# Kernel tuning notes

Hardware: AMD Instinct MI355X
Metric: run time of the kernel (lower is better)

Reference implementation:

```python
import jax, jax.numpy as jnp
import numpy as np

B, R, D, P = 32, 512, 256, 5532  # images, rois/image, feat dim, num_pids
NEG_INF = -1e30

def setup_inputs() -> dict:
    key = jax.random.key(0)
    k1, k2, k3 = jax.random.split(key, 3)
    inputs = jax.random.normal(k1, (B * R, D), dtype=jnp.float32)
    cls_scores = jax.random.uniform(k2, (B * R, 1), dtype=jnp.float32)
    roi_label = jax.random.randint(k3, (B, R), 0, P + 1)  # 0 = background -> label -1
    return {"inputs": inputs, "cls_scores": cls_scores, "roi_label": roi_label}

def reference(inputs, cls_scores, roi_label):
    x = (inputs * cls_scores).reshape(B, R, D)          # scale features by cls score
    label = roi_label - 1                               # [B,R], -1 = background
    valid = label >= 0                                  # keep labeled ROIs only
    lbl = jnp.where(valid, label, 0)

    # per-image per-pid mean prototypes via one segmented reduction
    seg = (jnp.arange(B)[:, None] * P + lbl).reshape(-1)             # [B*R]
    w = valid.reshape(-1).astype(x.dtype)
    sums = jax.ops.segment_sum(x.reshape(-1, D) * w[:, None], seg, num_segments=B * P)
    counts = jax.ops.segment_sum(w, seg, num_segments=B * P)          # [B*P]
    proto = sums / jnp.maximum(counts, 1.0)[:, None]
    proto = proto / jnp.maximum(jnp.linalg.norm(proto, axis=-1, keepdims=True), 1e-12)
    proto = jax.lax.stop_gradient(proto).reshape(B, P, D)            # .detach() in torch
    present = (counts > 0).reshape(B, P)                              # unique labels per image

    # project each ROI feature onto its image's prototypes
    logits = jnp.einsum('brd,bpd->brp', x, proto)                     # [B,R,P]
    logits = jnp.where(present[:, None, :], logits, NEG_INF)          # softmax over unique labels only
    logp = jax.nn.log_softmax(logits, axis=-1)
    nll = -jnp.take_along_axis(logp, lbl[..., None], axis=-1)[..., 0] # [B,R]
    nll = jnp.where(valid, nll, 0.0)
    n_valid = jnp.maximum(jnp.sum(valid).astype(x.dtype), 1.0)
    return jnp.sum(nll) / n_valid
```

## Files before the change

### kernel.cpp

```cpp
#include <hip/hip_runtime.h>
#include <math.h>

#define Bn 32
#define Rn 512
#define Dn 256
#define Pn 5532
#define MAXU 512

typedef short short8 __attribute__((ext_vector_type(8)));
typedef short short4v __attribute__((ext_vector_type(4)));
typedef float floatx4 __attribute__((ext_vector_type(4)));

#define XBF_OFF    0
#define XBF_WORDS  (Bn*Rn*Dn/2)
#define PBF_OFF    (XBF_OFF + XBF_WORDS)
#define PBF_WORDS  (Bn*MAXU*Dn/2)
#define LBLC_OFF   (PBF_OFF + PBF_WORDS)
#define CCNT_OFF   (LBLC_OFF + Bn*Rn)
#define CURS_OFF   (CCNT_OFF + Bn*MAXU)
#define RLIST_OFF  (CURS_OFF + Bn*MAXU)
#define NUNIQ_OFF  (RLIST_OFF + Bn*Rn)
#define NVALID_OFF (NUNIQ_OFF + 32)
#define NLL_OFF    (NVALID_OFF + 32)
#define TICK_OFF   (NLL_OFF + 1)
#define ZEROW      2

__device__ __forceinline__ unsigned short bf16r(float f) {
    union { float f; unsigned int u; } c; c.f = f;
    return (unsigned short)((c.u + 0x7FFFu + ((c.u >> 16) & 1u)) >> 16);
}
__device__ __forceinline__ float bfu2f(unsigned int hi16) {
    union { unsigned int u; float f; } c; c.u = hi16;
    return c.f;
}

__device__ __forceinline__ void async16(void* lds, const void* g) {
    auto* l3 = reinterpret_cast<__attribute__((address_space(3))) unsigned int*>(
                   reinterpret_cast<size_t>(lds));
    auto* g1 = reinterpret_cast<const __attribute__((address_space(1))) unsigned int*>(
                   reinterpret_cast<size_t>(g));
    __builtin_amdgcn_global_load_lds(g1, l3, 16, 0, 0);
}

__global__ __launch_bounds__(1024) void k1_prep(
    const float* __restrict__ inputs, const float* __restrict__ cls,
    const int* __restrict__ roi_label,
    unsigned short* __restrict__ xbf,
    int* __restrict__ lblc_arr, int* __restrict__ ccnt, int* __restrict__ cursor,
    int* __restrict__ rlist, int* __restrict__ nuniq, int* __restrict__ nvalid_arr,
    int* __restrict__ zbase)
{
    const int flat = blockIdx.x;
    const int t = threadIdx.x;

    __shared__ int cnt_lds[Pn];
    __shared__ int cmap_lds[Pn];
    __shared__ int curs_lds[MAXU];
    __shared__ int wpres[16], wcnt[16];

    if (flat >= 32) {
        if (flat == 33 && t < ZEROW) zbase[t] = 0;
        int g = (flat - 32) * 1024 + t;
        int e = g * 8;
        int row = e >> 8;
        float cw = cls[row];
        float4 v0 = *(const float4*)&inputs[e];
        float4 v1 = *(const float4*)&inputs[e + 4];
        short8 o;
        o[0] = (short)bf16r(v0.x * cw); o[1] = (short)bf16r(v0.y * cw);
        o[2] = (short)bf16r(v0.z * cw); o[3] = (short)bf16r(v0.w * cw);
        o[4] = (short)bf16r(v1.x * cw); o[5] = (short)bf16r(v1.y * cw);
        o[6] = (short)bf16r(v1.z * cw); o[7] = (short)bf16r(v1.w * cw);
        *(short8*)&xbf[e] = o;
        return;
    }

    const int b = flat;
    const int lane = t & 63, wid = t >> 6;
    for (int i = t; i < Pn; i += 1024) cnt_lds[i] = 0;
    __syncthreads();
    int mylbl = -1;
    if (t < Rn) {
        mylbl = roi_label[b * Rn + t] - 1;
        if (mylbl >= 0) atomicAdd(&cnt_lds[mylbl], 1);
    }
    __syncthreads();

    int basePres = 0, baseCnt = 0;
    for (int i0 = 0; i0 < Pn; i0 += 1024) {
        int i = i0 + t;
        int cnt = (i < Pn) ? cnt_lds[i] : 0;
        bool pres = cnt > 0;
        unsigned long long mask = __ballot(pres);
        int pfx_pres = __popcll(mask & ((1ULL << lane) - 1ULL));
        int v = cnt;
        #pragma unroll
        for (int off = 1; off < 64; off <<= 1) {
            int u = __shfl_up(v, off);
            if (lane >= off) v += u;
        }
        int pfx_cnt = v - cnt;
        if (lane == 63) { wpres[wid] = __popcll(mask); wcnt[wid] = v; }
        __syncthreads();
        int woffP = 0, totP = 0, woffC = 0, totC = 0;
        #pragma unroll
        for (int w = 0; w < 16; ++w) {
            int p = wpres[w], c = wcnt[w];
            if (w < wid) { woffP += p; woffC += c; }
            totP += p; totC += c;
        }
        if (pres) {
            int c = basePres + woffP + pfx_pres;
            cmap_lds[i] = c;
            ccnt[b * MAXU + c] = cnt;
            curs_lds[c] = baseCnt + woffC + pfx_cnt;
        }
        basePres += totP; baseCnt += totC;
        __syncthreads();
    }
    if (t < Rn) {
        int lc = (mylbl >= 0) ? cmap_lds[mylbl] : -1;
        lblc_arr[b * Rn + t] = lc;
        if (lc >= 0) {
            int pos = atomicAdd(&curs_lds[lc], 1);
            rlist[b * Rn + pos] = t;
        }
    }
    __syncthreads();
    if (t < MAXU && t < basePres)
        cursor[b * MAXU + t] = curs_lds[t];
    if (t == 0) { nuniq[b] = basePres; nvalid_arr[b] = baseCnt; }
}

__global__ __launch_bounds__(256) void k2_proto(
    const unsigned short* __restrict__ xbf,
    const int* __restrict__ nuniq, const int* __restrict__ ccnt,
    const int* __restrict__ cursor, const int* __restrict__ rlist,
    unsigned short* __restrict__ pbf)
{
    const int lane = threadIdx.x & 63, wv = threadIdx.x >> 6;
    int s = blockIdx.x * 4 + wv;
    int b = s >> 9;
    int c = s & (MAXU - 1);
    if (c >= nuniq[b]) return;
    int cnt = ccnt[s];
    int start = cursor[s] - cnt;
    float a0 = 0.f, a1 = 0.f, a2 = 0.f, a3 = 0.f;
    for (int k = 0; k < cnt; ++k) {
        int r = rlist[b * Rn + start + k];
        uint2 pk = *(const uint2*)&xbf[((size_t)(b * Rn + r)) * Dn + lane * 4];
        a0 += bfu2f(pk.x << 16); a1 += bfu2f(pk.x & 0xFFFF0000u);
        a2 += bfu2f(pk.y << 16); a3 += bfu2f(pk.y & 0xFFFF0000u);
    }
    float inv = 1.0f / (float)cnt;
    a0 *= inv; a1 *= inv; a2 *= inv; a3 *= inv;
    float ss = a0*a0 + a1*a1 + a2*a2 + a3*a3;
    #pragma unroll
    for (int off = 32; off > 0; off >>= 1) ss += __shfl_xor(ss, off);
    float scale = 1.0f / fmaxf(sqrtf(ss), 1e-12f);
    short4v o;
    o[0] = (short)bf16r(a0 * scale); o[1] = (short)bf16r(a1 * scale);
    o[2] = (short)bf16r(a2 * scale); o[3] = (short)bf16r(a3 * scale);
    *(short4v*)&pbf[(size_t)s * Dn + lane * 4] = o;
}

#define TRr 32
#define TCc 128
#define KCs 64
#define NSTG (Dn / KCs)
#define NBLK ((Rn / TRr) * Bn)

__global__ __launch_bounds__(256, 3) void k3_loss(
    const unsigned short* __restrict__ xbf, const unsigned short* __restrict__ pbf,
    const int* __restrict__ lblc_arr, const int* __restrict__ nuniq,
    const int* __restrict__ nvalid_arr,
    float* __restrict__ nll, int* __restrict__ tick, float* __restrict__ out)
{
    __shared__ __align__(16) unsigned short xs[TRr * Dn];
    __shared__ __align__(16) unsigned short ps[2][TCc * KCs];
    __shared__ int lblc[TRr];
    __shared__ float esum_lds[4][TRr];
    __shared__ float dsum_lds[4][TRr];

    const int t = threadIdx.x;
    const int lane = t & 63, w = t >> 6;
    const int q = lane >> 4, r15 = lane & 15;
    const int rt = blockIdx.x;
    const int b  = blockIdx.y;
    const int roiBase = rt * TRr;
    const int U = nuniq[b];
    const int nch = (U <= 0) ? 1 : ((U + TCc - 1) >> 7);

    if (t < TRr) lblc[t] = lblc_arr[b * Rn + roiBase + t];

    #pragma unroll
    for (int i = 0; i < 4; ++i) {
        int ci = i * 256 + w * 64 + lane;
        int row = ci >> 5, gpos = ci & 31;
        int g = gpos ^ (row & 7);
        async16(&xs[(i * 256 + w * 64) * 8],
                xbf + (size_t)(b * Rn + roiBase + row) * Dn + g * 8);
    }

#define ISSUE_PS(PC, ST, BUF)                                                \
    do {                                                                     \
        _Pragma("unroll")                                                    \
        for (int i_ = 0; i_ < 4; ++i_) {                                     \
            int ci_ = i_ * 256 + w * 64 + lane;                              \
            int pr_ = ci_ >> 3, gp_ = ci_ & 7;                               \
            int g_ = gp_ ^ (pr_ & 7);                                        \
            async16(&ps[BUF][(i_ * 256 + w * 64) * 8],                       \
                    pbf + (size_t)(b * MAXU + (PC) * TCc + pr_) * Dn         \
                        + (ST) * KCs + g_ * 8);                              \
        }                                                                    \
    } while (0)

    ISSUE_PS(0, 0, 0);
    __syncthreads();

    short8 areg[2][8];
    #pragma unroll
    for (int mt = 0; mt < 2; ++mt)
        #pragma unroll
        for (int kcs = 0; kcs < 8; ++kcs) {
            int row = mt * 16 + r15;
            int gpos = (kcs * 4 + q) ^ (row & 7);
            areg[mt][kcs] = *(const short8*)&xs[row * Dn + gpos * 8];
        }

    int lcr[2][4];
    float esum[2][4], dsum[2][4];
    #pragma unroll
    for (int mt = 0; mt < 2; ++mt)
        #pragma unroll
        for (int reg = 0; reg < 4; ++reg) {
            lcr[mt][reg] = lblc[mt * 16 + q * 4 + reg];
            esum[mt][reg] = 0.f; dsum[mt][reg] = 0.f;
        }

    for (int pc = 0; pc < nch; ++pc) {
        floatx4 acc[2][2];
        #pragma unroll
        for (int mt = 0; mt < 2; ++mt) {
            acc[mt][0] = (floatx4)0.f; acc[mt][1] = (floatx4)0.f;
        }

        #pragma unroll
        for (int st = 0; st < NSTG; ++st) {
            const int cur = st & 1;
            __syncthreads();
            int ns = pc * NSTG + st + 1;
            if (ns < nch * NSTG) ISSUE_PS(ns >> 2, ns & 3, cur ^ 1);
            #pragma unroll
            for (int kk = 0; kk < 2; ++kk) {
                short8 bb[2];
                #pragma unroll
                for (int nt = 0; nt < 2; ++nt) {
                    int r = w * 32 + nt * 16 + r15;
                    int gpos = (kk * 4 + q) ^ (r & 7);
                    bb[nt] = *(const short8*)&ps[cur][r * KCs + gpos * 8];
                }
                #pragma unroll
                for (int mt = 0; mt < 2; ++mt) {
                    acc[mt][0] = __builtin_amdgcn_mfma_f32_16x16x32_bf16(
                        areg[mt][st * 2 + kk], bb[0], acc[mt][0], 0, 0, 0);
                    acc[mt][1] = __builtin_amdgcn_mfma_f32_16x16x32_bf16(
                        areg[mt][st * 2 + kk], bb[1], acc[mt][1], 0, 0, 0);
                }
            }
        }

        #pragma unroll
        for (int nt = 0; nt < 2; ++nt) {
            int c = pc * TCc + w * 32 + nt * 16 + r15;
            bool v = c < U;
            #pragma unroll
            for (int mt = 0; mt < 2; ++mt)
                #pragma unroll
                for (int reg = 0; reg < 4; ++reg) {
                    float d = acc[mt][nt][reg];
                    if (v) esum[mt][reg] += __expf(d);
                    if (c == lcr[mt][reg]) dsum[mt][reg] += d;
                }
        }
    }
#undef ISSUE_PS

    #pragma unroll
    for (int mt = 0; mt < 2; ++mt)
        #pragma unroll
        for (int reg = 0; reg < 4; ++reg) {
            float e = esum[mt][reg], d = dsum[mt][reg];
            #pragma unroll
            for (int off = 1; off < 16; off <<= 1) {
                e += __shfl_xor(e, off);
                d += __shfl_xor(d, off);
            }
            if (r15 == 0) {
                int row = mt * 16 + q * 4 + reg;
                esum_lds[w][row] = e;
                dsum_lds[w][row] = d;
            }
        }
    __syncthreads();
    if (t < TRr) {
        float es = esum_lds[0][t] + esum_lds[1][t] + esum_lds[2][t] + esum_lds[3][t];
        float ds = dsum_lds[0][t] + dsum_lds[1][t] + dsum_lds[2][t] + dsum_lds[3][t];
        float val = (lblc[t] >= 0) ? (__logf(es) - ds) : 0.f;
        #pragma unroll
        for (int off = 1; off < 32; off <<= 1) val += __shfl_xor(val, off);
        if (t == 0) {
            atomicAdd(nll, val);
            __threadfence();
            int old = atomicAdd(tick, 1);
            if (old == NBLK - 1) {
                float total = atomicAdd(nll, 0.0f);
                int nv = 0;
                #pragma unroll
                for (int i = 0; i < Bn / 4; ++i) {
                    int4 vv = ((const int4*)nvalid_arr)[i];
                    nv += vv.x + vv.y + vv.z + vv.w;
                }
                out[0] = total / fmaxf((float)nv, 1.0f);
            }
        }
    }
}

extern "C" void kernel_launch(void* const* d_in, const int* in_sizes, int n_in,
                              void* d_out, int out_size, void* d_ws, size_t ws_size,
                              hipStream_t stream) {
    const float* inputs = (const float*)d_in[0];
    const float* cls    = (const float*)d_in[1];
    const int*   roi    = (const int*)d_in[2];
    float* out = (float*)d_out;

    float* wsf = (float*)d_ws;
    int*   wsi = (int*)d_ws;
    unsigned short* xbf = (unsigned short*)(wsi + XBF_OFF);
    unsigned short* pbf = (unsigned short*)(wsi + PBF_OFF);
    int*   lblc   = wsi + LBLC_OFF;
    int*   ccnt   = wsi + CCNT_OFF;
    int*   cursor = wsi + CURS_OFF;
    int*   rlist  = wsi + RLIST_OFF;
    int*   nuniq  = wsi + NUNIQ_OFF;
    int*   nvalid = wsi + NVALID_OFF;
    float* nll    = wsf + NLL_OFF;
    int*   tick   = wsi + TICK_OFF;

    k1_prep<<<32 + 512, 1024, 0, stream>>>(inputs, cls, roi, xbf, lblc, ccnt,
                                           cursor, rlist, nuniq, nvalid,
                                           wsi + NLL_OFF);
    k2_proto<<<(Bn * MAXU) / 4, 256, 0, stream>>>(xbf, nuniq, ccnt, cursor,
                                                  rlist, pbf);
    dim3 g(Rn / TRr, Bn);
    k3_loss<<<g, 256, 0, stream>>>(xbf, pbf, lblc, nuniq, nvalid, nll, tick, out);
}
```

Before: 104.9 us.

## Fuse prep, prototype and loss kernels into one persistent kernel with grid barriers

Merges the three launches into a single persistent kernel of 512 blocks. Stages are separated by a software grid barrier built on atomics. The bf16 scaled-feature buffer is no longer written to global memory: prototypes and loss tiles recompute the cls-scaled bf16 values straight from the fp32 inputs. Label compaction now assigns slots by first-arrival atomics instead of a prefix scan over all pids. This removes launch gaps and the intermediate round trip, at the cost of barrier spin overhead, a co-residency requirement for all 512 blocks, and only 32 blocks doing the prep stage.

Result: slower. 191.3 us (+82.4%).

```diff
diff --git a/kernel.cpp b/kernel.cpp
--- a/kernel.cpp
+++ b/kernel.cpp
@@ -6,14 +6,15 @@
 #define Dn 256
 #define Pn 5532
 #define MAXU 512
-
-typedef short short8 __attribute__((ext_vector_type(8)));
-typedef short short4v __attribute__((ext_vector_type(4)));
-typedef float floatx4 __attribute__((ext_vector_type(4)));
-
-#define XBF_OFF    0
-#define XBF_WORDS  (Bn*Rn*Dn/2)
-#define PBF_OFF    (XBF_OFF + XBF_WORDS)
+#define GRID 512
+
+#define TRr 32
+#define TCc 128
+#define KCs 64
+#define NSTG (Dn / KCs)
+#define NBLK GRID
+
+#define PBF_OFF    0
 #define PBF_WORDS  (Bn*MAXU*Dn/2)
 #define LBLC_OFF   (PBF_OFF + PBF_WORDS)
 #define CCNT_OFF   (LBLC_OFF + Bn*Rn)
@@ -23,7 +24,11 @@
 #define NVALID_OFF (NUNIQ_OFF + 32)
 #define NLL_OFF    (NVALID_OFF + 32)
 #define TICK_OFF   (NLL_OFF + 1)
-#define ZEROW      2
+#define BAR_OFF    (TICK_OFF + 1)
+
+typedef short short8 __attribute__((ext_vector_type(8)));
+typedef short short4v __attribute__((ext_vector_type(4)));
+typedef float floatx4 __attribute__((ext_vector_type(4)));
 
 __device__ __forceinline__ unsigned short bf16r(float f) {
     union { float f; unsigned int u; } c; c.f = f;
@@ -42,165 +47,161 @@
     __builtin_amdgcn_global_load_lds(g1, l3, 16, 0, 0);
 }
 
-__global__ __launch_bounds__(1024) void k1_prep(
-    const float* __restrict__ inputs, const float* __restrict__ cls,
-    const int* __restrict__ roi_label,
-    unsigned short* __restrict__ xbf,
-    int* __restrict__ lblc_arr, int* __restrict__ ccnt, int* __restrict__ cursor,
-    int* __restrict__ rlist, int* __restrict__ nuniq, int* __restrict__ nvalid_arr,
-    int* __restrict__ zbase)
-{
-    const int flat = blockIdx.x;
-    const int t = threadIdx.x;
-
-    __shared__ int cnt_lds[Pn];
-    __shared__ int cmap_lds[Pn];
-    __shared__ int curs_lds[MAXU];
-    __shared__ int wpres[16], wcnt[16];
-
-    if (flat >= 32) {
-        if (flat == 33 && t < ZEROW) zbase[t] = 0;
-        int g = (flat - 32) * 1024 + t;
-        int e = g * 8;
-        int row = e >> 8;
-        float cw = cls[row];
-        float4 v0 = *(const float4*)&inputs[e];
-        float4 v1 = *(const float4*)&inputs[e + 4];
-        short8 o;
-        o[0] = (short)bf16r(v0.x * cw); o[1] = (short)bf16r(v0.y * cw);
-        o[2] = (short)bf16r(v0.z * cw); o[3] = (short)bf16r(v0.w * cw);
-        o[4] = (short)bf16r(v1.x * cw); o[5] = (short)bf16r(v1.y * cw);
-        o[6] = (short)bf16r(v1.z * cw); o[7] = (short)bf16r(v1.w * cw);
-        *(short8*)&xbf[e] = o;
-        return;
-    }
-
-    const int b = flat;
-    const int lane = t & 63, wid = t >> 6;
-    for (int i = t; i < Pn; i += 1024) cnt_lds[i] = 0;
+__device__ __forceinline__ void gbar(int* bar, int target) {
     __syncthreads();
-    int mylbl = -1;
-    if (t < Rn) {
-        mylbl = roi_label[b * Rn + t] - 1;
-        if (mylbl >= 0) atomicAdd(&cnt_lds[mylbl], 1);
+    if (threadIdx.x == 0) {
+        __threadfence();
+        atomicAdd(bar, 1);
+        while (atomicAdd(bar, 0) < target)
+            __builtin_amdgcn_s_sleep(8);
+        __threadfence();
     }
     __syncthreads();
-
-    int basePres = 0, baseCnt = 0;
-    for (int i0 = 0; i0 < Pn; i0 += 1024) {
-        int i = i0 + t;
-        int cnt = (i < Pn) ? cnt_lds[i] : 0;
-        bool pres = cnt > 0;
-        unsigned long long mask = __ballot(pres);
-        int pfx_pres = __popcll(mask & ((1ULL << lane) - 1ULL));
-        int v = cnt;
-        #pragma unroll
-        for (int off = 1; off < 64; off <<= 1) {
-            int u = __shfl_up(v, off);
-            if (lane >= off) v += u;
-        }
-        int pfx_cnt = v - cnt;
-        if (lane == 63) { wpres[wid] = __popcll(mask); wcnt[wid] = v; }
-        __syncthreads();
-        int woffP = 0, totP = 0, woffC = 0, totC = 0;
-        #pragma unroll
-        for (int w = 0; w < 16; ++w) {
-            int p = wpres[w], c = wcnt[w];
-            if (w < wid) { woffP += p; woffC += c; }
-            totP += p; totC += c;
-        }
-        if (pres) {
-            int c = basePres + woffP + pfx_pres;
-            cmap_lds[i] = c;
-            ccnt[b * MAXU + c] = cnt;
-            curs_lds[c] = baseCnt + woffC + pfx_cnt;
-        }
-        basePres += totP; baseCnt += totC;
-        __syncthreads();
+}
+
+__global__ __launch_bounds__(256, 2) void fused(
+    const float* __restrict__ inputs, const float* __restrict__ cls,
+    const int* __restrict__ roi_label, int* __restrict__ wsi,
+    float* __restrict__ out)
+{
+    __shared__ __align__(16) char smem[50432];
+
+    const int t = threadIdx.x;
+    const int blk = blockIdx.x;
+    const int lane = t & 63, wv = t >> 6;
+
+    unsigned short* pbf = (unsigned short*)(wsi + PBF_OFF);
+    int* lblc_arr = wsi + LBLC_OFF;
+    int* ccnt     = wsi + CCNT_OFF;
+    int* cursor   = wsi + CURS_OFF;
+    int* rlist    = wsi + RLIST_OFF;
+    int* nuniq    = wsi + NUNIQ_OFF;
+    int* nvalid_a = wsi + NVALID_OFF;
+    float* nll    = (float*)(wsi + NLL_OFF);
+    int* tick     = wsi + TICK_OFF;
+    int* bar      = wsi + BAR_OFF;
+
+    if (blk < Bn) {
+        int* cnt_l  = (int*)smem;
+        int* slot_l = cnt_l + Pn;
+        int* scnt   = slot_l + Pn;
+        int* sbase  = scnt + MAXU;
+        int* scur   = sbase + MAXU;
+        int* ctrs   = scur + MAXU;
+        const int b = blk;
+        for (int i = t; i < Pn; i += 256) cnt_l[i] = 0;
+        for (int i = t; i < MAXU; i += 256) scnt[i] = 0;
+        if (t == 0) ctrs[0] = 0;
+        __syncthreads();
+        int myl[2], mylc[2];
+        #pragma unroll
+        for (int j = 0; j < 2; ++j) {
+            int l = roi_label[b * Rn + t + j * 256] - 1;
+            myl[j] = l;
+            if (l >= 0) {
+                if (atomicAdd(&cnt_l[l], 1) == 0)
+                    slot_l[l] = atomicAdd(&ctrs[0], 1);
+            }
+        }
+        __syncthreads();
+        #pragma unroll
+        for (int j = 0; j < 2; ++j) {
+            int lc = (myl[j] >= 0) ? slot_l[myl[j]] : -1;
+            mylc[j] = lc;
+            lblc_arr[b * Rn + t + j * 256] = lc;
+            if (lc >= 0) atomicAdd(&scnt[lc], 1);
+        }
+        __syncthreads();
+        const int U = ctrs[0];
+        int base = 0;
+        for (int i0 = 0; i0 < MAXU; i0 += 256) {
+            int v = scnt[i0 + t], vs = v;
+            #pragma unroll
+            for (int off = 1; off < 64; off <<= 1) {
+                int u = __shfl_up(vs, off);
+                if (lane >= off) vs += u;
+            }
+            if (lane == 63) ctrs[2 + wv] = vs;
+            __syncthreads();
+            int woff = 0, tot = 0;
+            #pragma unroll
+            for (int w = 0; w < 4; ++w) {
+                int x = ctrs[2 + w];
+                if (w < wv) woff += x;
+                tot += x;
+            }
+            int st = base + woff + (vs - v);
+            sbase[i0 + t] = st;
+            scur[i0 + t]  = st;
+            base += tot;
+            __syncthreads();
+        }
+        #pragma unroll
+        for (int j = 0; j < 2; ++j) {
+            int lc = mylc[j];
+            if (lc >= 0) {
+                int pos = atomicAdd(&scur[lc], 1);
+                rlist[b * Rn + pos] = t + j * 256;
+            }
+        }
+        __syncthreads();
+        for (int i = t; i < MAXU; i += 256)
+            if (i < U) { ccnt[b*MAXU+i] = scnt[i]; cursor[b*MAXU+i] = sbase[i]; }
+        if (t == 0) { nuniq[b] = U; nvalid_a[b] = base; }
     }
-    if (t < Rn) {
-        int lc = (mylbl >= 0) ? cmap_lds[mylbl] : -1;
-        lblc_arr[b * Rn + t] = lc;
-        if (lc >= 0) {
-            int pos = atomicAdd(&curs_lds[lc], 1);
-            rlist[b * Rn + pos] = t;
+
+    gbar(bar, GRID);
+
+    {
+        const int gs0 = blk * 32 + wv * 8;
+        const int b = gs0 >> 9;
+        const int Ub = nuniq[b];
+        for (int i = 0; i < 8; ++i) {
+            int c = (gs0 + i) & (MAXU - 1);
+            if (c >= Ub) continue;
+            int s = b * MAXU + c;
+            int cnt = ccnt[s], start = cursor[s];
+            float a0 = 0.f, a1 = 0.f, a2 = 0.f, a3 = 0.f;
+            for (int k = 0; k < cnt; ++k) {
+                int row = b * Rn + rlist[b * Rn + start + k];
+                float cw = cls[row];
+                float4 v = *(const float4*)&inputs[(size_t)row * Dn + lane * 4];
+                a0 += bfu2f(((unsigned)bf16r(v.x * cw)) << 16);
+                a1 += bfu2f(((unsigned)bf16r(v.y * cw)) << 16);
+                a2 += bfu2f(((unsigned)bf16r(v.z * cw)) << 16);
+                a3 += bfu2f(((unsigned)bf16r(v.w * cw)) << 16);
+            }
+            float inv = 1.0f / (float)cnt;
+            a0 *= inv; a1 *= inv; a2 *= inv; a3 *= inv;
+            float ss = a0*a0 + a1*a1 + a2*a2 + a3*a3;
+            #pragma unroll
+            for (int off = 32; off > 0; off >>= 1) ss += __shfl_xor(ss, off);
+            float sc = 1.0f / fmaxf(sqrtf(ss), 1e-12f);
+            short4v o;
+            o[0] = (short)bf16r(a0 * sc); o[1] = (short)bf16r(a1 * sc);
+            o[2] = (short)bf16r(a2 * sc); o[3] = (short)bf16r(a3 * sc);
+            *(short4v*)&pbf[(size_t)s * Dn + lane * 4] = o;
         }
     }
-    __syncthreads();
-    if (t < MAXU && t < basePres)
-        cursor[b * MAXU + t] = curs_lds[t];
-    if (t == 0) { nuniq[b] = basePres; nvalid_arr[b] = baseCnt; }
-}
-
-__global__ __launch_bounds__(256) void k2_proto(
-    const unsigned short* __restrict__ xbf,
-    const int* __restrict__ nuniq, const int* __restrict__ ccnt,
-    const int* __restrict__ cursor, const int* __restrict__ rlist,
-    unsigned short* __restrict__ pbf)
-{
-    const int lane = threadIdx.x & 63, wv = threadIdx.x >> 6;
-    int s = blockIdx.x * 4 + wv;
-    int b = s >> 9;
-    int c = s & (MAXU - 1);
-    if (c >= nuniq[b]) return;
-    int cnt = ccnt[s];
-    int start = cursor[s] - cnt;
-    float a0 = 0.f, a1 = 0.f, a2 = 0.f, a3 = 0.f;
-    for (int k = 0; k < cnt; ++k) {
-        int r = rlist[b * Rn + start + k];
-        uint2 pk = *(const uint2*)&xbf[((size_t)(b * Rn + r)) * Dn + lane * 4];
-        a0 += bfu2f(pk.x << 16); a1 += bfu2f(pk.x & 0xFFFF0000u);
-        a2 += bfu2f(pk.y << 16); a3 += bfu2f(pk.y & 0xFFFF0000u);
-    }
-    float inv = 1.0f / (float)cnt;
-    a0 *= inv; a1 *= inv; a2 *= inv; a3 *= inv;
-    float ss = a0*a0 + a1*a1 + a2*a2 + a3*a3;
-    #pragma unroll
-    for (int off = 32; off > 0; off >>= 1) ss += __shfl_xor(ss, off);
-    float scale = 1.0f / fmaxf(sqrtf(ss), 1e-12f);
-    short4v o;
-    o[0] = (short)bf16r(a0 * scale); o[1] = (short)bf16r(a1 * scale);
-    o[2] = (short)bf16r(a2 * scale); o[3] = (short)bf16r(a3 * scale);
-    *(short4v*)&pbf[(size_t)s * Dn + lane * 4] = o;
-}
-
-#define TRr 32
-#define TCc 128
-#define KCs 64
-#define NSTG (Dn / KCs)
-#define NBLK ((Rn / TRr) * Bn)
-
-__global__ __launch_bounds__(256, 3) void k3_loss(
-    const unsigned short* __restrict__ xbf, const unsigned short* __restrict__ pbf,
-    const int* __restrict__ lblc_arr, const int* __restrict__ nuniq,
-    const int* __restrict__ nvalid_arr,
-    float* __restrict__ nll, int* __restrict__ tick, float* __restrict__ out)
-{
-    __shared__ __align__(16) unsigned short xs[TRr * Dn];
-    __shared__ __align__(16) unsigned short ps[2][TCc * KCs];
-    __shared__ int lblc[TRr];
-    __shared__ float esum_lds[4][TRr];
-    __shared__ float dsum_lds[4][TRr];
-
-    const int t = threadIdx.x;
-    const int lane = t & 63, w = t >> 6;
-    const int q = lane >> 4, r15 = lane & 15;
-    const int rt = blockIdx.x;
-    const int b  = blockIdx.y;
-    const int roiBase = rt * TRr;
-    const int U = nuniq[b];
-    const int nch = (U <= 0) ? 1 : ((U + TCc - 1) >> 7);
-
-    if (t < TRr) lblc[t] = lblc_arr[b * Rn + roiBase + t];
-
-    #pragma unroll
-    for (int i = 0; i < 4; ++i) {
-        int ci = i * 256 + w * 64 + lane;
-        int row = ci >> 5, gpos = ci & 31;
-        int g = gpos ^ (row & 7);
-        async16(&xs[(i * 256 + w * 64) * 8],
-                xbf + (size_t)(b * Rn + roiBase + row) * Dn + g * 8);
-    }
+
+    gbar(bar, 2 * GRID);
+
+    {
+        unsigned short* xs  = (unsigned short*)smem;
+        unsigned short* psb = xs + TRr * Dn;
+        int*   lblc = (int*)(psb + 2 * TCc * KCs);
+        float* es_l = (float*)(lblc + TRr);
+        float* ds_l = es_l + 4 * TRr;
+
+        const int w = wv;
+        const int q = lane >> 4, r15 = lane & 15;
+        const int rt = blk & 15;
+        const int b  = blk >> 4;
+        const int roiBase = rt * TRr;
+        const int U = nuniq[b];
+        const int nch = (U <= 0) ? 1 : ((U + TCc - 1) >> 7);
+
+        if (t < TRr) lblc[t] = lblc_arr[b * Rn + roiBase + t];
 
 #define ISSUE_PS(PC, ST, BUF)                                                \
     do {                                                                     \
@@ -209,119 +210,140 @@
             int ci_ = i_ * 256 + w * 64 + lane;                              \
             int pr_ = ci_ >> 3, gp_ = ci_ & 7;                               \
             int g_ = gp_ ^ (pr_ & 7);                                        \
-            async16(&ps[BUF][(i_ * 256 + w * 64) * 8],                       \
+            async16(psb + (size_t)(BUF) * (TCc * KCs)                        \
+                        + (size_t)(i_ * 256 + w * 64) * 8,                   \
                     pbf + (size_t)(b * MAXU + (PC) * TCc + pr_) * Dn         \
                         + (ST) * KCs + g_ * 8);                              \
         }                                                                    \
     } while (0)
 
-    ISSUE_PS(0, 0, 0);
-    __syncthreads();
-
-    short8 areg[2][8];
-    #pragma unroll
-    for (int mt = 0; mt < 2; ++mt)
-        #pragma unroll
-        for (int kcs = 0; kcs < 8; ++kcs) {
-            int row = mt * 16 + r15;
-            int gpos = (kcs * 4 + q) ^ (row & 7);
-            areg[mt][kcs] = *(const short8*)&xs[row * Dn + gpos * 8];
-        }
-
-    int lcr[2][4];
-    float esum[2][4], dsum[2][4];
-    #pragma unroll
-    for (int mt = 0; mt < 2; ++mt)
-        #pragma unroll
-        for (int reg = 0; reg < 4; ++reg) {
-            lcr[mt][reg] = lblc[mt * 16 + q * 4 + reg];
-            esum[mt][reg] = 0.f; dsum[mt][reg] = 0.f;
-        }
-
-    for (int pc = 0; pc < nch; ++pc) {
-        floatx4 acc[2][2];
-        #pragma unroll
-        for (int mt = 0; mt < 2; ++mt) {
-            acc[mt][0] = (floatx4)0.f; acc[mt][1] = (floatx4)0.f;
-        }
-
-        #pragma unroll
-        for (int st = 0; st < NSTG; ++st) {
-            const int cur = st & 1;
-            __syncthreads();
-            int ns = pc * NSTG + st + 1;
-            if (ns < nch * NSTG) ISSUE_PS(ns >> 2, ns & 3, cur ^ 1);
-            #pragma unroll
-            for (int kk = 0; kk < 2; ++kk) {
-                short8 bb[2];
+        ISSUE_PS(0, 0, 0);
+
+        {
+            const int row = t >> 3, seg = t & 7;
+            const size_t gbase = (size_t)(b * Rn + roiBase + row) * Dn + seg * 32;
+            const float cw = cls[b * Rn + roiBase + row];
+            #pragma unroll
+            for (int jj = 0; jj < 4; ++jj) {
+                float4 v0 = *(const float4*)&inputs[gbase + jj * 8];
+                float4 v1 = *(const float4*)&inputs[gbase + jj * 8 + 4];
+                short8 o;
+                o[0] = (short)bf16r(v0.x * cw); o[1] = (short)bf16r(v0.y * cw);
+                o[2] = (short)bf16r(v0.z * cw); o[3] = (short)bf16r(v0.w * cw);
+                o[4] = (short)bf16r(v1.x * cw); o[5] = (short)bf16r(v1.y * cw);
+                o[6] = (short)bf16r(v1.z * cw); o[7] = (short)bf16r(v1.w * cw);
+                int gpos = (seg * 4 + jj) ^ (row & 7);
+                *(short8*)&xs[row * Dn + gpos * 8] = o;
+            }
+        }
+        __syncthreads();
+
+        short8 areg[2][8];
+        #pragma unroll
+        for (int mt = 0; mt < 2; ++mt)
+            #pragma unroll
+            for (int kcs = 0; kcs < 8; ++kcs) {
+                int row = mt * 16 + r15;
+                int gpos = (kcs * 4 + q) ^ (row & 7);
+                areg[mt][kcs] = *(const short8*)&xs[row * Dn + gpos * 8];
+            }
+
+        int lcr[2][4];
+        float esum[2][4], dsum[2][4];
+        #pragma unroll
+        for (int mt = 0; mt < 2; ++mt)
+            #pragma unroll
+            for (int reg = 0; reg < 4; ++reg) {
+                lcr[mt][reg] = lblc[mt * 16 + q * 4 + reg];
+                esum[mt][reg] = 0.f; dsum[mt][reg] = 0.f;
+            }
+
+        for (int pc = 0; pc < nch; ++pc) {
+            floatx4 acc[2][2];
+            #pragma unroll
+            for (int mt = 0; mt < 2; ++mt) {
+                acc[mt][0] = (floatx4)0.f; acc[mt][1] = (floatx4)0.f;
+            }
+
+            #pragma unroll
+            for (int st = 0; st < NSTG; ++st) {
+                const int cur = st & 1;
+                __syncthreads();
+                int ns = pc * NSTG + st + 1;
+                if (ns < nch * NSTG) ISSUE_PS(ns >> 2, ns & 3, cur ^ 1);
+                const unsigned short* pscur = psb + (size_t)cur * (TCc * KCs);
                 #pragma unroll
-                for (int nt = 0; nt < 2; ++nt) {
-                    int r = w * 32 + nt * 16 + r15;
-                    int gpos = (kk * 4 + q) ^ (r & 7);
-                    bb[nt] = *(const short8*)&ps[cur][r * KCs + gpos * 8];
+                for (int kk = 0; kk < 2; ++kk) {
+                    short8 bb[2];
+                    #pragma unroll
+                    for (int nt = 0; nt < 2; ++nt) {
+                        int r = w * 32 + nt * 16 + r15;
+                        int gpos = (kk * 4 + q) ^ (r & 7);
+                        bb[nt] = *(const short8*)&pscur[r * KCs + gpos * 8];
+                    }
+                    #pragma unroll
+                    for (int mt = 0; mt < 2; ++mt) {
+                        acc[mt][0] = __builtin_amdgcn_mfma_f32_16x16x32_bf16(
+                            areg[mt][st * 2 + kk], bb[0], acc[mt][0], 0, 0, 0);
+                        acc[mt][1] = __builtin_amdgcn_mfma_f32_16x16x32_bf16(
+                            areg[mt][st * 2 + kk], bb[1], acc[mt][1], 0, 0, 0);
+                    }
                 }
+            }
+
+            #pragma unroll
+            for (int nt = 0; nt < 2; ++nt) {
+                int c = pc * TCc + w * 32 + nt * 16 + r15;
+                bool v = c < U;
                 #pragma unroll
-                for (int mt = 0; mt < 2; ++mt) {
-                    acc[mt][0] = __builtin_amdgcn_mfma_f32_16x16x32_bf16(
-                        areg[mt][st * 2 + kk], bb[0], acc[mt][0], 0, 0, 0);
-                    acc[mt][1] = __builtin_amdgcn_mfma_f32_16x16x32_bf16(
-                        areg[mt][st * 2 + kk], bb[1], acc[mt][1], 0, 0, 0);
+                for (int mt = 0; mt < 2; ++mt)
+                    #pragma unroll
+                    for (int reg = 0; reg < 4; ++reg) {
+                        float d = acc[mt][nt][reg];
+                        if (v) esum[mt][reg] += __expf(d);
+                        if (c == lcr[mt][reg]) dsum[mt][reg] += d;
+                    }
+            }
+        }
+#undef ISSUE_PS
+
+        #pragma unroll
+        for (int mt = 0; mt < 2; ++mt)
+            #pragma unroll
+            for (int reg = 0; reg < 4; ++reg) {
+                float e = esum[mt][reg], d = dsum[mt][reg];
+                #pragma unroll
+                for (int off = 1; off < 16; off <<= 1) {
+                    e += __shfl_xor(e, off);
+                    d += __shfl_xor(d, off);
                 }
-            }
-        }
-
-        #pragma unroll
-        for (int nt = 0; nt < 2; ++nt) {
-            int c = pc * TCc + w * 32 + nt * 16 + r15;
-            bool v = c < U;
-            #pragma unroll
-            for (int mt = 0; mt < 2; ++mt)
-                #pragma unroll
-                for (int reg = 0; reg < 4; ++reg) {
-                    float d = acc[mt][nt][reg];
-                    if (v) esum[mt][reg] += __expf(d);
-                    if (c == lcr[mt][reg]) dsum[mt][reg] += d;
+                if (r15 == 0) {
+                    int row = mt * 16 + q * 4 + reg;
+                    es_l[w * TRr + row] = e;
+                    ds_l[w * TRr + row] = d;
                 }
-        }
-    }
-#undef ISSUE_PS
-
-    #pragma unroll
-    for (int mt = 0; mt < 2; ++mt)
-        #pragma unroll
-        for (int reg = 0; reg < 4; ++reg) {
-            float e = esum[mt][reg], d = dsum[mt][reg];
-            #pragma unroll
-            for (int off = 1; off < 16; off <<= 1) {
-                e += __shfl_xor(e, off);
-                d += __shfl_xor(d, off);
-            }
-            if (r15 == 0) {
-                int row = mt * 16 + q * 4 + reg;
-                esum_lds[w][row] = e;
-                dsum_lds[w][row] = d;
-            }
-        }
-    __syncthreads();
-    if (t < TRr) {
-        float es = esum_lds[0][t] + esum_lds[1][t] + esum_lds[2][t] + esum_lds[3][t];
-        float ds = dsum_lds[0][t] + dsum_lds[1][t] + dsum_lds[2][t] + dsum_lds[3][t];
-        float val = (lblc[t] >= 0) ? (__logf(es) - ds) : 0.f;
-        #pragma unroll
-        for (int off = 1; off < 32; off <<= 1) val += __shfl_xor(val, off);
-        if (t == 0) {
-            atomicAdd(nll, val);
-            __threadfence();
-            int old = atomicAdd(tick, 1);
-            if (old == NBLK - 1) {
-                float total = atomicAdd(nll, 0.0f);
-                int nv = 0;
-                #pragma unroll
-                for (int i = 0; i < Bn / 4; ++i) {
-                    int4 vv = ((const int4*)nvalid_arr)[i];
-                    nv += vv.x + vv.y + vv.z + vv.w;
+            }
+        __syncthreads();
+        if (t < TRr) {
+            float es = es_l[t] + es_l[TRr + t] + es_l[2*TRr + t] + es_l[3*TRr + t];
+            float ds = ds_l[t] + ds_l[TRr + t] + ds_l[2*TRr + t] + ds_l[3*TRr + t];
+            float val = (lblc[t] >= 0) ? (__logf(es) - ds) : 0.f;
+            #pragma unroll
+            for (int off = 1; off < 32; off <<= 1) val += __shfl_xor(val, off);
+            if (t == 0) {
+                atomicAdd(nll, val);
+                __threadfence();
+                int old = atomicAdd(tick, 1);
+                if (old == NBLK - 1) {
+                    float total = atomicAdd(nll, 0.0f);
+                    int nv = 0;
+                    #pragma unroll
+                    for (int i = 0; i < Bn / 4; ++i) {
+                        int4 vv = ((const int4*)nvalid_a)[i];
+                        nv += vv.x + vv.y + vv.z + vv.w;
+                    }
+                    out[0] = total / fmaxf((float)nv, 1.0f);
                 }
-                out[0] = total / fmaxf((float)nv, 1.0f);
             }
         }
     }
@@ -333,26 +355,9 @@
     const float* inputs = (const float*)d_in[0];
     const float* cls    = (const float*)d_in[1];
     const int*   roi    = (const int*)d_in[2];
+    int* wsi   = (int*)d_ws;
     float* out = (float*)d_out;
 
-    float* wsf = (float*)d_ws;
-    int*   wsi = (int*)d_ws;
-    unsigned short* xbf = (unsigned short*)(wsi + XBF_OFF);
-    unsigned short* pbf = (unsigned short*)(wsi + PBF_OFF);
-    int*   lblc   = wsi + LBLC_OFF;
-    int*   ccnt   = wsi + CCNT_OFF;
-    int*   cursor = wsi + CURS_OFF;
-    int*   rlist  = wsi + RLIST_OFF;
-    int*   nuniq  = wsi + NUNIQ_OFF;
-    int*   nvalid = wsi + NVALID_OFF;
-    float* nll    = wsf + NLL_OFF;
-    int*   tick   = wsi + TICK_OFF;
-
-    k1_prep<<<32 + 512, 1024, 0, stream>>>(inputs, cls, roi, xbf, lblc, ccnt,
-                                           cursor, rlist, nuniq, nvalid,
-                                           wsi + NLL_OFF);
-    k2_proto<<<(Bn * MAXU) / 4, 256, 0, stream>>>(xbf, nuniq, ccnt, cursor,
-                                                  rlist, pbf);
-    dim3 g(Rn / TRr, Bn);
-    k3_loss<<<g, 256, 0, stream>>>(xbf, pbf, lblc, nuniq, nvalid, nll, tick, out);
-}
+    hipMemsetAsync((char*)d_ws + (size_t)NLL_OFF * 4, 0, 12, stream);
+    fused<<<GRID, 256, 0, stream>>>(inputs, cls, roi, wsi, out);
+}
```

## Fuse prototype building into prep kernel and drop bf16 feature staging buffer

Applied to the files above, without the earlier changes.

Merges the label-compaction and prototype-mean kernels into one per-image kernel that keeps counts, cursors and ROI lists in LDS and reads fp32 inputs directly. The loss kernel now scales and converts its ROI tile to bf16 itself instead of loading a precomputed bf16 copy, and its launch-bounds occupancy hint changes from 3 to 2 blocks per CU. This removes one launch and the global round trip through the bf16 feature, list and cursor buffers. The cost is that prototype work now runs on only 32 blocks, which limits parallelism, and fp32 inputs are read twice.

After: 126.8 us. +20.9%, slower.

```diff
diff --git a/kernel.cpp b/kernel.cpp
--- a/kernel.cpp
+++ b/kernel.cpp
@@ -7,23 +7,23 @@
 #define Pn 5532
 #define MAXU 512
 
+#define TRr 32
+#define TCc 128
+#define KCs 64
+#define NSTG (Dn / KCs)
+#define NBLK ((Rn / TRr) * Bn)
+
+#define PBF_OFF    0
+#define PBF_WORDS  (Bn*MAXU*Dn/2)
+#define LBLC_OFF   (PBF_OFF + PBF_WORDS)
+#define NUNIQ_OFF  (LBLC_OFF + Bn*Rn)
+#define NVALID_OFF (NUNIQ_OFF + 32)
+#define NLL_OFF    (NVALID_OFF + 32)
+#define TICK_OFF   (NLL_OFF + 1)
+
 typedef short short8 __attribute__((ext_vector_type(8)));
 typedef short short4v __attribute__((ext_vector_type(4)));
 typedef float floatx4 __attribute__((ext_vector_type(4)));
-
-#define XBF_OFF    0
-#define XBF_WORDS  (Bn*Rn*Dn/2)
-#define PBF_OFF    (XBF_OFF + XBF_WORDS)
-#define PBF_WORDS  (Bn*MAXU*Dn/2)
-#define LBLC_OFF   (PBF_OFF + PBF_WORDS)
-#define CCNT_OFF   (LBLC_OFF + Bn*Rn)
-#define CURS_OFF   (CCNT_OFF + Bn*MAXU)
-#define RLIST_OFF  (CURS_OFF + Bn*MAXU)
-#define NUNIQ_OFF  (RLIST_OFF + Bn*Rn)
-#define NVALID_OFF (NUNIQ_OFF + 32)
-#define NLL_OFF    (NVALID_OFF + 32)
-#define TICK_OFF   (NLL_OFF + 1)
-#define ZEROW      2
 
 __device__ __forceinline__ unsigned short bf16r(float f) {
     union { float f; unsigned int u; } c; c.f = f;
@@ -42,41 +42,26 @@
     __builtin_amdgcn_global_load_lds(g1, l3, 16, 0, 0);
 }
 
-__global__ __launch_bounds__(1024) void k1_prep(
+__global__ __launch_bounds__(1024) void k12_prep_proto(
     const float* __restrict__ inputs, const float* __restrict__ cls,
     const int* __restrict__ roi_label,
-    unsigned short* __restrict__ xbf,
-    int* __restrict__ lblc_arr, int* __restrict__ ccnt, int* __restrict__ cursor,
-    int* __restrict__ rlist, int* __restrict__ nuniq, int* __restrict__ nvalid_arr,
-    int* __restrict__ zbase)
+    unsigned short* __restrict__ pbf, int* __restrict__ lblc_arr,
+    int* __restrict__ nuniq, int* __restrict__ nvalid_arr,
+    int* __restrict__ zwords)
 {
-    const int flat = blockIdx.x;
-    const int t = threadIdx.x;
-
     __shared__ int cnt_lds[Pn];
     __shared__ int cmap_lds[Pn];
     __shared__ int curs_lds[MAXU];
+    __shared__ int scnt_lds[MAXU];
+    __shared__ int rl_lds[Rn];
     __shared__ int wpres[16], wcnt[16];
 
-    if (flat >= 32) {
-        if (flat == 33 && t < ZEROW) zbase[t] = 0;
-        int g = (flat - 32) * 1024 + t;
-        int e = g * 8;
-        int row = e >> 8;
-        float cw = cls[row];
-        float4 v0 = *(const float4*)&inputs[e];
-        float4 v1 = *(const float4*)&inputs[e + 4];
-        short8 o;
-        o[0] = (short)bf16r(v0.x * cw); o[1] = (short)bf16r(v0.y * cw);
-        o[2] = (short)bf16r(v0.z * cw); o[3] = (short)bf16r(v0.w * cw);
-        o[4] = (short)bf16r(v1.x * cw); o[5] = (short)bf16r(v1.y * cw);
-        o[6] = (short)bf16r(v1.z * cw); o[7] = (short)bf16r(v1.w * cw);
-        *(short8*)&xbf[e] = o;
-        return;
-    }
-
-    const int b = flat;
+    const int b = blockIdx.x;
+    const int t = threadIdx.x;
     const int lane = t & 63, wid = t >> 6;
+
+    if (b == 0 && t == 0) { zwords[0] = 0; zwords[1] = 0; }
+
     for (int i = t; i < Pn; i += 1024) cnt_lds[i] = 0;
     __syncthreads();
     int mylbl = -1;
@@ -112,7 +97,7 @@
         if (pres) {
             int c = basePres + woffP + pfx_pres;
             cmap_lds[i] = c;
-            ccnt[b * MAXU + c] = cnt;
+            scnt_lds[c] = cnt;
             curs_lds[c] = baseCnt + woffC + pfx_cnt;
         }
         basePres += totP; baseCnt += totC;
@@ -123,64 +108,76 @@
         lblc_arr[b * Rn + t] = lc;
         if (lc >= 0) {
             int pos = atomicAdd(&curs_lds[lc], 1);
-            rlist[b * Rn + pos] = t;
-        }
-    }
-    __syncthreads();
-    if (t < MAXU && t < basePres)
-        cursor[b * MAXU + t] = curs_lds[t];
+            rl_lds[pos] = t;
+        }
+    }
     if (t == 0) { nuniq[b] = basePres; nvalid_arr[b] = baseCnt; }
-}
-
-__global__ __launch_bounds__(256) void k2_proto(
-    const unsigned short* __restrict__ xbf,
-    const int* __restrict__ nuniq, const int* __restrict__ ccnt,
-    const int* __restrict__ cursor, const int* __restrict__ rlist,
-    unsigned short* __restrict__ pbf)
-{
-    const int lane = threadIdx.x & 63, wv = threadIdx.x >> 6;
-    int s = blockIdx.x * 4 + wv;
-    int b = s >> 9;
-    int c = s & (MAXU - 1);
-    if (c >= nuniq[b]) return;
-    int cnt = ccnt[s];
-    int start = cursor[s] - cnt;
-    float a0 = 0.f, a1 = 0.f, a2 = 0.f, a3 = 0.f;
-    for (int k = 0; k < cnt; ++k) {
-        int r = rlist[b * Rn + start + k];
-        uint2 pk = *(const uint2*)&xbf[((size_t)(b * Rn + r)) * Dn + lane * 4];
-        a0 += bfu2f(pk.x << 16); a1 += bfu2f(pk.x & 0xFFFF0000u);
-        a2 += bfu2f(pk.y << 16); a3 += bfu2f(pk.y & 0xFFFF0000u);
-    }
-    float inv = 1.0f / (float)cnt;
-    a0 *= inv; a1 *= inv; a2 *= inv; a3 *= inv;
-    float ss = a0*a0 + a1*a1 + a2*a2 + a3*a3;
-    #pragma unroll
-    for (int off = 32; off > 0; off >>= 1) ss += __shfl_xor(ss, off);
-    float scale = 1.0f / fmaxf(sqrtf(ss), 1e-12f);
-    short4v o;
-    o[0] = (short)bf16r(a0 * scale); o[1] = (short)bf16r(a1 * scale);
-    o[2] = (short)bf16r(a2 * scale); o[3] = (short)bf16r(a3 * scale);
-    *(short4v*)&pbf[(size_t)s * Dn + lane * 4] = o;
-}
-
-#define TRr 32
-#define TCc 128
-#define KCs 64
-#define NSTG (Dn / KCs)
-#define NBLK ((Rn / TRr) * Bn)
-
-__global__ __launch_bounds__(256, 3) void k3_loss(
-    const unsigned short* __restrict__ xbf, const unsigned short* __restrict__ pbf,
+    __syncthreads();
+    const int U = basePres;
+
+    for (int cb = wid; cb < U; cb += 64) {
+        int cntj[4], stj[4];
+        #pragma unroll
+        for (int j = 0; j < 4; ++j) {
+            int c = cb + 16 * j;
+            bool ok = c < U;
+            int cnt = ok ? scnt_lds[c] : 0;
+            cntj[j] = cnt;
+            stj[j]  = ok ? (curs_lds[c] - cnt) : 0;
+        }
+        int rj[4];
+        #pragma unroll
+        for (int j = 0; j < 4; ++j) rj[j] = cntj[j] ? rl_lds[stj[j]] : 0;
+        float cwj[4]; float4 vj[4];
+        #pragma unroll
+        for (int j = 0; j < 4; ++j) {
+            int row = b * Rn + rj[j];
+            cwj[j] = cls[row];
+            vj[j]  = *(const float4*)&inputs[(size_t)row * Dn + lane * 4];
+        }
+        #pragma unroll
+        for (int j = 0; j < 4; ++j) {
+            if (!cntj[j]) continue;
+            float a0 = bfu2f(((unsigned)bf16r(vj[j].x * cwj[j])) << 16);
+            float a1 = bfu2f(((unsigned)bf16r(vj[j].y * cwj[j])) << 16);
+            float a2 = bfu2f(((unsigned)bf16r(vj[j].z * cwj[j])) << 16);
+            float a3 = bfu2f(((unsigned)bf16r(vj[j].w * cwj[j])) << 16);
+            for (int k = 1; k < cntj[j]; ++k) {
+                int row = b * Rn + rl_lds[stj[j] + k];
+                float cw = cls[row];
+                float4 v = *(const float4*)&inputs[(size_t)row * Dn + lane * 4];
+                a0 += bfu2f(((unsigned)bf16r(v.x * cw)) << 16);
+                a1 += bfu2f(((unsigned)bf16r(v.y * cw)) << 16);
+                a2 += bfu2f(((unsigned)bf16r(v.z * cw)) << 16);
+                a3 += bfu2f(((unsigned)bf16r(v.w * cw)) << 16);
+            }
+            float inv = 1.0f / (float)cntj[j];
+            a0 *= inv; a1 *= inv; a2 *= inv; a3 *= inv;
+            float ss = a0*a0 + a1*a1 + a2*a2 + a3*a3;
+            #pragma unroll
+            for (int off = 32; off > 0; off >>= 1) ss += __shfl_xor(ss, off);
+            float sc = 1.0f / fmaxf(sqrtf(ss), 1e-12f);
+            short4v o;
+            o[0] = (short)bf16r(a0 * sc); o[1] = (short)bf16r(a1 * sc);
+            o[2] = (short)bf16r(a2 * sc); o[3] = (short)bf16r(a3 * sc);
+            int s = b * MAXU + cb + 16 * j;
+            *(short4v*)&pbf[(size_t)s * Dn + lane * 4] = o;
+        }
+    }
+}
+
+__global__ __launch_bounds__(256, 2) void k3_loss(
+    const float* __restrict__ inputs, const float* __restrict__ cls,
+    const unsigned short* __restrict__ pbf,
     const int* __restrict__ lblc_arr, const int* __restrict__ nuniq,
     const int* __restrict__ nvalid_arr,
     float* __restrict__ nll, int* __restrict__ tick, float* __restrict__ out)
 {
     __shared__ __align__(16) unsigned short xs[TRr * Dn];
-    __shared__ __align__(16) unsigned short ps[2][TCc * KCs];
+    __shared__ __align__(16) unsigned short psb[2][TCc * KCs];
     __shared__ int lblc[TRr];
-    __shared__ float esum_lds[4][TRr];
-    __shared__ float dsum_lds[4][TRr];
+    __shared__ float es_l[4][TRr];
+    __shared__ float ds_l[4][TRr];
 
     const int t = threadIdx.x;
     const int lane = t & 63, w = t >> 6;
@@ -193,15 +190,6 @@
 
     if (t < TRr) lblc[t] = lblc_arr[b * Rn + roiBase + t];
 
-    #pragma unroll
-    for (int i = 0; i < 4; ++i) {
-        int ci = i * 256 + w * 64 + lane;
-        int row = ci >> 5, gpos = ci & 31;
-        int g = gpos ^ (row & 7);
-        async16(&xs[(i * 256 + w * 64) * 8],
-                xbf + (size_t)(b * Rn + roiBase + row) * Dn + g * 8);
-    }
-
 #define ISSUE_PS(PC, ST, BUF)                                                \
     do {                                                                     \
         _Pragma("unroll")                                                    \
@@ -209,13 +197,31 @@
             int ci_ = i_ * 256 + w * 64 + lane;                              \
             int pr_ = ci_ >> 3, gp_ = ci_ & 7;                               \
             int g_ = gp_ ^ (pr_ & 7);                                        \
-            async16(&ps[BUF][(i_ * 256 + w * 64) * 8],                       \
+            async16(&psb[BUF][(i_ * 256 + w * 64) * 8],                      \
                     pbf + (size_t)(b * MAXU + (PC) * TCc + pr_) * Dn         \
                         + (ST) * KCs + g_ * 8);                              \
         }                                                                    \
     } while (0)
 
     ISSUE_PS(0, 0, 0);
+
+    {
+        const int row = t >> 3, seg = t & 7;
+        const size_t gbase = (size_t)(b * Rn + roiBase + row) * Dn + seg * 32;
+        const float cw = cls[b * Rn + roiBase + row];
+        #pragma unroll
+        for (int jj = 0; jj < 4; ++jj) {
+            float4 v0 = *(const float4*)&inputs[gbase + jj * 8];
+            float4 v1 = *(const float4*)&inputs[gbase + jj * 8 + 4];
+            short8 o;
+            o[0] = (short)bf16r(v0.x * cw); o[1] = (short)bf16r(v0.y * cw);
+            o[2] = (short)bf16r(v0.z * cw); o[3] = (short)bf16r(v0.w * cw);
+            o[4] = (short)bf16r(v1.x * cw); o[5] = (short)bf16r(v1.y * cw);
+            o[6] = (short)bf16r(v1.z * cw); o[7] = (short)bf16r(v1.w * cw);
+            int gpos = (seg * 4 + jj) ^ (row & 7);
+            *(short8*)&xs[row * Dn + gpos * 8] = o;
+        }
+    }
     __syncthreads();
 
     short8 areg[2][8];
@@ -258,7 +264,7 @@
                 for (int nt = 0; nt < 2; ++nt) {
                     int r = w * 32 + nt * 16 + r15;
                     int gpos = (kk * 4 + q) ^ (r & 7);
-                    bb[nt] = *(const short8*)&ps[cur][r * KCs + gpos * 8];
+                    bb[nt] = *(const short8*)&psb[cur][r * KCs + gpos * 8];
                 }
                 #pragma unroll
                 for (int mt = 0; mt < 2; ++mt) {
@@ -298,14 +304,14 @@
             }
             if (r15 == 0) {
                 int row = mt * 16 + q * 4 + reg;
-                esum_lds[w][row] = e;
-                dsum_lds[w][row] = d;
+                es_l[w][row] = e;
+                ds_l[w][row] = d;
             }
         }
     __syncthreads();
     if (t < TRr) {
-        float es = esum_lds[0][t] + esum_lds[1][t] + esum_lds[2][t] + esum_lds[3][t];
-        float ds = dsum_lds[0][t] + dsum_lds[1][t] + dsum_lds[2][t] + dsum_lds[3][t];
+        float es = es_l[0][t] + es_l[1][t] + es_l[2][t] + es_l[3][t];
+        float ds = ds_l[0][t] + ds_l[1][t] + ds_l[2][t] + ds_l[3][t];
         float val = (lblc[t] >= 0) ? (__logf(es) - ds) : 0.f;
         #pragma unroll
         for (int off = 1; off < 32; off <<= 1) val += __shfl_xor(val, off);
@@ -333,26 +339,19 @@
     const float* inputs = (const float*)d_in[0];
     const float* cls    = (const float*)d_in[1];
     const int*   roi    = (const int*)d_in[2];
+    int* wsi   = (int*)d_ws;
     float* out = (float*)d_out;
 
-    float* wsf = (float*)d_ws;
-    int*   wsi = (int*)d_ws;
-    unsigned short* xbf = (unsigned short*)(wsi + XBF_OFF);
     unsigned short* pbf = (unsigned short*)(wsi + PBF_OFF);
     int*   lblc   = wsi + LBLC_OFF;
-    int*   ccnt   = wsi + CCNT_OFF;
-    int*   cursor = wsi + CURS_OFF;
-    int*   rlist  = wsi + RLIST_OFF;
     int*   nuniq  = wsi + NUNIQ_OFF;
     int*   nvalid = wsi + NVALID_OFF;
-    float* nll    = wsf + NLL_OFF;
+    float* nll    = (float*)(wsi + NLL_OFF);
     int*   tick   = wsi + TICK_OFF;
 
-    k1_prep<<<32 + 512, 1024, 0, stream>>>(inputs, cls, roi, xbf, lblc, ccnt,
-                                           cursor, rlist, nuniq, nvalid,
-                                           wsi + NLL_OFF);
-    k2_proto<<<(Bn * MAXU) / 4, 256, 0, stream>>>(xbf, nuniq, ccnt, cursor,
-                                                  rlist, pbf);
+    k12_prep_proto<<<Bn, 1024, 0, stream>>>(inputs, cls, roi, pbf, lblc,
+                                            nuniq, nvalid, wsi + NLL_OFF);
     dim3 g(Rn / TRr, Bn);
-    k3_loss<<<g, 256, 0, stream>>>(xbf, pbf, lblc, nuniq, nvalid, nll, tick, out);
-}
+    k3_loss<<<g, 256, 0, stream>>>(inputs, cls, pbf, lblc, nuniq, nvalid,
+                                   nll, tick, out);
+}
```
